# Kernel optimization log

Measured on AMD Instinct MI355X. Metric: run time of the kernel, lower is better.

## Reference

```python
import jax, jax.numpy as jnp
import numpy as np

T, H, I, BS = 512, 4096, 11008, 128


def _dequant(w, scale, bs):
    # w: [I, H], scale: [I//bs, H//bs] -> w * blockwise-broadcast scale
    Iw, Hw = w.shape
    wb = w.reshape(Iw // bs, bs, Hw // bs, bs)
    return (wb * scale[:, None, :, None]).reshape(Iw, Hw)


def setup_inputs() -> dict:
    key = jax.random.key(0)
    ks = jax.random.split(key, 7)
    return {
        "x": jax.random.normal(ks[0], (T, H), dtype=jnp.float32),
        "gate_weight": jax.random.normal(ks[1], (I, H), dtype=jnp.float32) * 0.02,
        "up_weight": jax.random.normal(ks[2], (I, H), dtype=jnp.float32) * 0.02,
        "down_weight": jax.random.normal(ks[3], (I, H), dtype=jnp.float32) * 0.02,
        "gate_scale": jax.random.uniform(ks[4], (I // BS, H // BS), dtype=jnp.float32),
        "up_scale": jax.random.uniform(ks[5], (I // BS, H // BS), dtype=jnp.float32),
        "down_scale": jax.random.uniform(ks[6], (I // BS, H // BS), dtype=jnp.float32),
        "blocksize": BS,
    }


def reference(x, gate_weight, up_weight, down_weight, gate_scale, up_scale, down_scale, blocksize):
    # Block-dequantize the three quantized weights, then SwiGLU MLP:
    # out = (silu(x @ Wg^T) * (x @ Wu^T)) @ Wd   (Wd stored pre-transposed as [I, H])
    wg = _dequant(gate_weight, gate_scale, blocksize)  # [I, H]
    wu = _dequant(up_weight, up_scale, blocksize)      # [I, H]
    wd = _dequant(down_weight, down_scale, blocksize)  # [I, H]
    gate = jnp.einsum('th,ih->ti', x, wg)  # [T, I]
    up = jnp.einsum('th,ih->ti', x, wu)    # [T, I]
    h = jax.nn.silu(gate) * up             # [T, I]
    return jnp.einsum('ti,ih->th', h, wd)  # [T, H]
```

## Files before the change

kernel.cpp:

```cpp
#include <hip/hip_runtime.h>
#include <hip/hip_bf16.h>
#include <cstdint>
#include <cstddef>

#define T_DIM 512
#define H_DIM 4096
#define I_DIM 11008
#define KSPLIT 4

typedef __bf16 bf16_t;
typedef bf16_t bf16x8 __attribute__((ext_vector_type(8)));
typedef float f32x4 __attribute__((ext_vector_type(4)));
typedef unsigned short us16;
typedef us16 us16x8 __attribute__((ext_vector_type(8)));
typedef us16 us16x4 __attribute__((ext_vector_type(4)));

__device__ __forceinline__ us16 f2bf(float f) {
    union { float f; uint32_t u; } v; v.f = f;
    uint32_t u = v.u;
    return (us16)((u + 0x7FFFu + ((u >> 16) & 1u)) >> 16);
}

__device__ __forceinline__ uint32_t pkbf(float a, float b) {
    __hip_bfloat162 h = __float22bfloat162_rn(make_float2(a, b));
    uint32_t u;
    __builtin_memcpy(&u, &h, 4);
    return u;
}

__device__ __forceinline__ f32x4 mfma16(us16x8 a, us16x8 b, f32x4 c) {
    return __builtin_amdgcn_mfma_f32_16x16x32_bf16(
        __builtin_bit_cast(bf16x8, a), __builtin_bit_cast(bf16x8, b), c, 0, 0, 0);
}

__device__ __forceinline__ void gload_lds16(const us16* g, us16* l) {
    __builtin_amdgcn_global_load_lds(
        (const __attribute__((address_space(1))) void*)g,
        (__attribute__((address_space(3))) void*)l, 16, 0, 0);
}

__global__ void cvt_x_kernel(const float* __restrict__ x, us16* __restrict__ xb) {
    int idx = (blockIdx.x * 256 + threadIdx.x) * 8;
    float4 a = *(const float4*)(x + idx);
    float4 b = *(const float4*)(x + idx + 4);
    us16x8 v;
    v[0] = f2bf(a.x); v[1] = f2bf(a.y); v[2] = f2bf(a.z); v[3] = f2bf(a.w);
    v[4] = f2bf(b.x); v[5] = f2bf(b.y); v[6] = f2bf(b.z); v[7] = f2bf(b.w);
    *(us16x8*)(xb + idx) = v;
}

__global__ __launch_bounds__(256) void trans_wd(
    const float* __restrict__ wd, const float* __restrict__ sd, us16* __restrict__ wdt)
{
    const int t   = threadIdx.x;
    const int bid = blockIdx.x;
    const int bi  = bid % (I_DIM / 256);
    const int bh  = bid / (I_DIM / 256);
    const int i   = bi * 256 + t;
    const int h0  = bh * 16;
    const float s = sd[(i >> 7) * (H_DIM / 128) + (h0 >> 7)];
    const float* src = wd + (size_t)i * H_DIM + h0;
    float4 v0 = *(const float4*)(src + 0);
    float4 v1 = *(const float4*)(src + 4);
    float4 v2 = *(const float4*)(src + 8);
    float4 v3 = *(const float4*)(src + 12);
    us16 o[16];
    o[0]=f2bf(v0.x*s); o[1]=f2bf(v0.y*s); o[2]=f2bf(v0.z*s); o[3]=f2bf(v0.w*s);
    o[4]=f2bf(v1.x*s); o[5]=f2bf(v1.y*s); o[6]=f2bf(v1.z*s); o[7]=f2bf(v1.w*s);
    o[8]=f2bf(v2.x*s); o[9]=f2bf(v2.y*s); o[10]=f2bf(v2.z*s); o[11]=f2bf(v2.w*s);
    o[12]=f2bf(v3.x*s); o[13]=f2bf(v3.y*s); o[14]=f2bf(v3.z*s); o[15]=f2bf(v3.w*s);
    #pragma unroll
    for (int j = 0; j < 16; ++j)
        wdt[(size_t)(h0 + j) * I_DIM + i] = o[j];
}

__global__ __launch_bounds__(256, 3) void gemm1_fused(
    const us16*  __restrict__ xb,
    const float* __restrict__ wg,
    const float* __restrict__ wu,
    const float* __restrict__ sgArr,
    const float* __restrict__ suArr,
    us16*        __restrict__ hbuf)
{
    __shared__ us16 As [128 * 72];
    __shared__ us16 Bgs[64 * 72];
    __shared__ us16 Bus[64 * 72];

    const int t    = threadIdx.x;
    const int bid  = blockIdx.x;
    const int wgid = (bid & 7) * 86 + (bid >> 3);
    const int bm   = wgid & 3;
    const int bn   = wgid >> 2;
    const int m0   = bm * 128, n0 = bn * 64;

    const int w = t >> 6, l = t & 63;
    const int q = l >> 4, r = l & 15;
    const int m_off = (w >> 1) * 64, n_off = (w & 1) * 32;

    const int ar[4] = { t >> 3, (t + 256) >> 3, (t + 512) >> 3, (t + 768) >> 3 };
    const int ac    = (t & 7) * 8;
    const int br[4] = { t >> 4, (t + 256) >> 4, (t + 512) >> 4, (t + 768) >> 4 };
    const int bc    = (t & 15) * 4;

    f32x4 accg[4][2], accu[4][2];
    #pragma unroll
    for (int m = 0; m < 4; ++m)
        #pragma unroll
        for (int n = 0; n < 2; ++n) {
            accg[m][n] = f32x4{0.f,0.f,0.f,0.f};
            accu[m][n] = f32x4{0.f,0.f,0.f,0.f};
        }

    us16x8 ab[4];
    float4 gb[4], ub[4];

    {
        const int k0 = 0;
        #pragma unroll
        for (int p = 0; p < 4; ++p)
            ab[p] = *(const us16x8*)(xb + (size_t)(m0 + ar[p]) * H_DIM + k0 + ac);
        #pragma unroll
        for (int p = 0; p < 4; ++p) {
            gb[p] = *(const float4*)(wg + (size_t)(n0 + br[p]) * H_DIM + k0 + bc);
            ub[p] = *(const float4*)(wu + (size_t)(n0 + br[p]) * H_DIM + k0 + bc);
        }
    }

    for (int kt = 0; kt < H_DIM / 64; ++kt) {
        const float sg = sgArr[(bn >> 1) * (H_DIM / 128) + (kt >> 1)];
        const float su = suArr[(bn >> 1) * (H_DIM / 128) + (kt >> 1)];

        __builtin_amdgcn_s_barrier();

        #pragma unroll
        for (int p = 0; p < 4; ++p)
            *(us16x8*)(As + ar[p] * 72 + ac) = ab[p];
        #pragma unroll
        for (int p = 0; p < 4; ++p) {
            uint2 vg, vu;
            vg.x = pkbf(gb[p].x * sg, gb[p].y * sg);
            vg.y = pkbf(gb[p].z * sg, gb[p].w * sg);
            vu.x = pkbf(ub[p].x * su, ub[p].y * su);
            vu.y = pkbf(ub[p].z * su, ub[p].w * su);
            *(uint2*)(Bgs + br[p] * 72 + bc) = vg;
            *(uint2*)(Bus + br[p] * 72 + bc) = vu;
        }

        {
            const int kn = ((kt + 1) & 63) * 64;
            #pragma unroll
            for (int p = 0; p < 4; ++p)
                ab[p] = *(const us16x8*)(xb + (size_t)(m0 + ar[p]) * H_DIM + kn + ac);
            #pragma unroll
            for (int p = 0; p < 4; ++p) {
                gb[p] = *(const float4*)(wg + (size_t)(n0 + br[p]) * H_DIM + kn + bc);
                ub[p] = *(const float4*)(wu + (size_t)(n0 + br[p]) * H_DIM + kn + bc);
            }
        }

        __builtin_amdgcn_s_waitcnt(0xC07F);
        __builtin_amdgcn_s_barrier();

        #pragma unroll
        for (int ks = 0; ks < 2; ++ks) {
            us16x8 af[4], bg[2], bu[2];
            #pragma unroll
            for (int m = 0; m < 4; ++m)
                af[m] = *(const us16x8*)(As + (m_off + m * 16 + r) * 72 + ks * 32 + q * 8);
            #pragma unroll
            for (int n = 0; n < 2; ++n) {
                bg[n] = *(const us16x8*)(Bgs + (n_off + n * 16 + r) * 72 + ks * 32 + q * 8);
                bu[n] = *(const us16x8*)(Bus + (n_off + n * 16 + r) * 72 + ks * 32 + q * 8);
            }
            #pragma unroll
            for (int m = 0; m < 4; ++m)
                #pragma unroll
                for (int n = 0; n < 2; ++n) {
                    accg[m][n] = mfma16(af[m], bg[n], accg[m][n]);
                    accu[m][n] = mfma16(af[m], bu[n], accu[m][n]);
                }
        }
    }

    #pragma unroll
    for (int m = 0; m < 4; ++m)
        #pragma unroll
        for (int n = 0; n < 2; ++n)
            #pragma unroll
            for (int rr = 0; rr < 4; ++rr) {
                int grow = m0 + m_off + m * 16 + q * 4 + rr;
                int gcol = n0 + n_off + n * 16 + r;
                float g = accg[m][n][rr];
                float u = accu[m][n][rr];
                float hv = (g / (1.0f + __expf(-g))) * u;
                hbuf[(size_t)grow * I_DIM + gcol] = f2bf(hv);
            }
}

template <bool USE_PART>
__global__ __launch_bounds__(256, 2) void gemm2_splitk(
    const us16* __restrict__ hbuf,
    const us16* __restrict__ wdt,
    float*      __restrict__ outp)
{
    __shared__ us16 As[128 * 32];
    __shared__ us16 Bs[128 * 32];

    const int t   = threadIdx.x;
    const int bid = blockIdx.x;
    const int x   = bid & 7;
    const int j   = bid >> 3;
    const int bm  = j & 3;
    const int g   = x * 16 + (j >> 2);
    const int bn  = g & 31;
    const int bk  = g >> 5;
    const int m0  = bm * 128, n0 = bn * 128;
    const int kbase = bk * (I_DIM / KSPLIT);

    const int w = t >> 6, l = t & 63;
    const int q = l >> 4, r = l & 15;
    const int m_off = (w >> 1) * 64, n_off = (w & 1) * 64;

    const int arow = w * 16 + (l >> 2);
    const int acol = (l & 3) * 8;

    f32x4 acc[4][4];
    #pragma unroll
    for (int m = 0; m < 4; ++m)
        #pragma unroll
        for (int n = 0; n < 4; ++n) acc[m][n] = f32x4{0.f,0.f,0.f,0.f};

    for (int kt = 0; kt < (I_DIM / KSPLIT) / 32; ++kt) {
        const int k0 = kbase + kt * 32;
        #pragma unroll
        for (int p = 0; p < 2; ++p) {
            gload_lds16(hbuf + (size_t)(m0 + p * 64 + arow) * I_DIM + k0 + acol,
                        As + (p * 64 + w * 16) * 32);
            gload_lds16(wdt + (size_t)(n0 + p * 64 + arow) * I_DIM + k0 + acol,
                        Bs + (p * 64 + w * 16) * 32);
        }
        __syncthreads();

        us16x8 af[4], bfr[4];
        #pragma unroll
        for (int m = 0; m < 4; ++m)
            af[m] = *(const us16x8*)(As + (m_off + m * 16 + r) * 32 + q * 8);
        #pragma unroll
        for (int n = 0; n < 4; ++n)
            bfr[n] = *(const us16x8*)(Bs + (n_off + n * 16 + r) * 32 + q * 8);
        #pragma unroll
        for (int m = 0; m < 4; ++m)
            #pragma unroll
            for (int n = 0; n < 4; ++n)
                acc[m][n] = mfma16(af[m], bfr[n], acc[m][n]);
        __syncthreads();
    }

    float* base = USE_PART ? outp + (size_t)bk * T_DIM * H_DIM : outp;
    #pragma unroll
    for (int m = 0; m < 4; ++m)
        #pragma unroll
        for (int n = 0; n < 4; ++n)
            #pragma unroll
            for (int rr = 0; rr < 4; ++rr) {
                int grow = m0 + m_off + m * 16 + q * 4 + rr;
                int gcol = n0 + n_off + n * 16 + r;
                if (USE_PART)
                    base[(size_t)grow * H_DIM + gcol] = acc[m][n][rr];
                else
                    atomicAdd(&base[(size_t)grow * H_DIM + gcol], acc[m][n][rr]);
            }
}

__global__ void reduce4_kernel(const float* __restrict__ part, float* __restrict__ out) {
    const size_t i = ((size_t)blockIdx.x * 256 + threadIdx.x) * 4;
    const size_t S = (size_t)T_DIM * H_DIM;
    float4 a = *(const float4*)(part + i);
    float4 b = *(const float4*)(part + S + i);
    float4 c = *(const float4*)(part + 2 * S + i);
    float4 d = *(const float4*)(part + 3 * S + i);
    float4 o;
    o.x = a.x + b.x + c.x + d.x;
    o.y = a.y + b.y + c.y + d.y;
    o.z = a.z + b.z + c.z + d.z;
    o.w = a.w + b.w + c.w + d.w;
    *(float4*)(out + i) = o;
}

extern "C" void kernel_launch(void* const* d_in, const int* in_sizes, int n_in,
                              void* d_out, int out_size, void* d_ws, size_t ws_size,
                              hipStream_t stream) {
    const float* x  = (const float*)d_in[0];
    const float* wg = (const float*)d_in[1];
    const float* wu = (const float*)d_in[2];
    const float* wd = (const float*)d_in[3];
    const float* sg = (const float*)d_in[4];
    const float* su = (const float*)d_in[5];
    const float* sd = (const float*)d_in[6];
    float* out = (float*)d_out;

    const size_t xb_bytes   = (size_t)T_DIM * H_DIM * 2;
    const size_t hb_bytes   = (size_t)T_DIM * I_DIM * 2;
    const size_t wdt_bytes  = (size_t)H_DIM * I_DIM * 2;
    const size_t part_bytes = (size_t)KSPLIT * T_DIM * H_DIM * 4;

    us16*  xb   = (us16*)d_ws;
    us16*  hb   = (us16*)((char*)d_ws + xb_bytes);
    us16*  wdt  = (us16*)((char*)d_ws + xb_bytes + hb_bytes);
    float* part = (float*)((char*)d_ws + xb_bytes + hb_bytes + wdt_bytes);

    cvt_x_kernel<<<(T_DIM * H_DIM) / (256 * 8), 256, 0, stream>>>(x, xb);
    gemm1_fused<<<(I_DIM / 64) * (T_DIM / 128), 256, 0, stream>>>(xb, wg, wu, sg, su, hb);
    trans_wd<<<(I_DIM / 256) * (H_DIM / 16), 256, 0, stream>>>(wd, sd, wdt);

    if (ws_size >= xb_bytes + hb_bytes + wdt_bytes + part_bytes) {
        gemm2_splitk<true><<<(T_DIM / 128) * (H_DIM / 128) * KSPLIT, 256, 0, stream>>>(hb, wdt, part);
        reduce4_kernel<<<(T_DIM * H_DIM) / (256 * 4), 256, 0, stream>>>(part, out);
    } else {
        (void)hipMemsetAsync(out, 0, (size_t)T_DIM * H_DIM * sizeof(float), stream);
        gemm2_splitk<false><<<(T_DIM / 128) * (H_DIM / 128) * KSPLIT, 256, 0, stream>>>(hb, wdt, out);
    }
}
```

Baseline: 666.3 us.

## Register-prefetch next K tile in gemm2 with padded 64-wide LDS tiles

Replaces the direct global-to-LDS loads in the down-projection GEMM with loads into registers that prefetch the next K tile while the current tile is consumed from LDS. The K step doubles from 32 to 64, and LDS rows are padded to 72 elements to avoid bank conflicts. This is meant to hide global memory latency and halve the number of barriers per K. In exchange it uses more registers and LDS, which may lower occupancy, and the final iteration issues a redundant wraparound prefetch.

```diff
diff --git a/kernel.cpp b/kernel.cpp
--- a/kernel.cpp
+++ b/kernel.cpp
@@ -31,12 +31,6 @@
 __device__ __forceinline__ f32x4 mfma16(us16x8 a, us16x8 b, f32x4 c) {
     return __builtin_amdgcn_mfma_f32_16x16x32_bf16(
         __builtin_bit_cast(bf16x8, a), __builtin_bit_cast(bf16x8, b), c, 0, 0, 0);
-}
-
-__device__ __forceinline__ void gload_lds16(const us16* g, us16* l) {
-    __builtin_amdgcn_global_load_lds(
-        (const __attribute__((address_space(1))) void*)g,
-        (__attribute__((address_space(3))) void*)l, 16, 0, 0);
 }
 
 __global__ void cvt_x_kernel(const float* __restrict__ x, us16* __restrict__ xb) {
@@ -203,15 +197,15 @@
     const us16* __restrict__ wdt,
     float*      __restrict__ outp)
 {
-    __shared__ us16 As[128 * 32];
-    __shared__ us16 Bs[128 * 32];
+    __shared__ us16 As[128 * 72];
+    __shared__ us16 Bs[128 * 72];
 
     const int t   = threadIdx.x;
     const int bid = blockIdx.x;
-    const int x   = bid & 7;
+    const int xcd = bid & 7;
     const int j   = bid >> 3;
     const int bm  = j & 3;
-    const int g   = x * 16 + (j >> 2);
+    const int g   = xcd * 16 + (j >> 2);
     const int bn  = g & 31;
     const int bk  = g >> 5;
     const int m0  = bm * 128, n0 = bn * 128;
@@ -221,8 +215,8 @@
     const int q = l >> 4, r = l & 15;
     const int m_off = (w >> 1) * 64, n_off = (w & 1) * 64;
 
-    const int arow = w * 16 + (l >> 2);
-    const int acol = (l & 3) * 8;
+    const int sr[4] = { t >> 3, (t >> 3) + 32, (t >> 3) + 64, (t >> 3) + 96 };
+    const int sc    = (t & 7) * 8;
 
     f32x4 acc[4][4];
     #pragma unroll
@@ -230,30 +224,55 @@
         #pragma unroll
         for (int n = 0; n < 4; ++n) acc[m][n] = f32x4{0.f,0.f,0.f,0.f};
 
-    for (int kt = 0; kt < (I_DIM / KSPLIT) / 32; ++kt) {
-        const int k0 = kbase + kt * 32;
-        #pragma unroll
-        for (int p = 0; p < 2; ++p) {
-            gload_lds16(hbuf + (size_t)(m0 + p * 64 + arow) * I_DIM + k0 + acol,
-                        As + (p * 64 + w * 16) * 32);
-            gload_lds16(wdt + (size_t)(n0 + p * 64 + arow) * I_DIM + k0 + acol,
-                        Bs + (p * 64 + w * 16) * 32);
-        }
-        __syncthreads();
-
-        us16x8 af[4], bfr[4];
-        #pragma unroll
-        for (int m = 0; m < 4; ++m)
-            af[m] = *(const us16x8*)(As + (m_off + m * 16 + r) * 32 + q * 8);
-        #pragma unroll
-        for (int n = 0; n < 4; ++n)
-            bfr[n] = *(const us16x8*)(Bs + (n_off + n * 16 + r) * 32 + q * 8);
-        #pragma unroll
-        for (int m = 0; m < 4; ++m)
+    us16x8 aReg[4], bReg[4];
+
+    {
+        const int k0 = kbase;
+        #pragma unroll
+        for (int p = 0; p < 4; ++p) {
+            aReg[p] = *(const us16x8*)(hbuf + (size_t)(m0 + sr[p]) * I_DIM + k0 + sc);
+            bReg[p] = *(const us16x8*)(wdt  + (size_t)(n0 + sr[p]) * I_DIM + k0 + sc);
+        }
+    }
+
+    const int NT = (I_DIM / KSPLIT) / 64;
+    for (int kt = 0; kt < NT; ++kt) {
+        __builtin_amdgcn_s_barrier();
+
+        #pragma unroll
+        for (int p = 0; p < 4; ++p) {
+            *(us16x8*)(As + sr[p] * 72 + sc) = aReg[p];
+            *(us16x8*)(Bs + sr[p] * 72 + sc) = bReg[p];
+        }
+
+        {
+            int ktn = kt + 1; if (ktn == NT) ktn = 0;
+            const int k0n = kbase + ktn * 64;
+            #pragma unroll
+            for (int p = 0; p < 4; ++p) {
+                aReg[p] = *(const us16x8*)(hbuf + (size_t)(m0 + sr[p]) * I_DIM + k0n + sc);
+                bReg[p] = *(const us16x8*)(wdt  + (size_t)(n0 + sr[p]) * I_DIM + k0n + sc);
+            }
+        }
+
+        __builtin_amdgcn_s_waitcnt(0xC07F);
+        __builtin_amdgcn_s_barrier();
+
+        #pragma unroll
+        for (int ks = 0; ks < 2; ++ks) {
+            us16x8 af[4], bfr[4];
+            #pragma unroll
+            for (int m = 0; m < 4; ++m)
+                af[m] = *(const us16x8*)(As + (m_off + m * 16 + r) * 72 + ks * 32 + q * 8);
             #pragma unroll
             for (int n = 0; n < 4; ++n)
-                acc[m][n] = mfma16(af[m], bfr[n], acc[m][n]);
-        __syncthreads();
+                bfr[n] = *(const us16x8*)(Bs + (n_off + n * 16 + r) * 72 + ks * 32 + q * 8);
+            #pragma unroll
+            for (int m = 0; m < 4; ++m)
+                #pragma unroll
+                for (int n = 0; n < 4; ++n)
+                    acc[m][n] = mfma16(af[m], bfr[n], acc[m][n]);
+        }
     }
 
     float* base = USE_PART ? outp + (size_t)bk * T_DIM * H_DIM : outp;
```

Result: faster. 643.4 us (-3.4%).
